# Kernel tuning notes

Hardware: AMD Instinct MI355X
Metric: run time of the kernel (lower is better)

## Reference

```python
import jax, jax.numpy as jnp
import numpy as np

HIDDEN = 512
IN_DIM = 512
N_ACT = 64
N_AGENTS = 8


def kalei_linear(x, ids, W, b, t):
    """x: [N, I]; ids: [N]; W: [O, I]; b: [O]; t: [A, O, I] -> [N, O].
    w_a = sign(W) * relu(|W| - sigmoid(t_a)); y_n = w_{ids[n]} @ x_n + b.
    """
    Wm = jnp.sign(W)[None] * jax.nn.relu(jnp.abs(W)[None] - jax.nn.sigmoid(t))  # [A,O,I]
    y = jnp.einsum('aoi,ni->nao', Wm, x)          # [N, A, O] batched masked GEMM
    y = jnp.take_along_axis(y, ids[:, None, None], axis=1)[:, 0]  # [N, O]
    return y + b[None, :]


def gru_cell(x, h, w_ih, w_hh, b_ih, b_hh):
    gi = x @ w_ih.T + b_ih
    gh = h @ w_hh.T + b_hh
    i_r, i_z, i_n = jnp.split(gi, 3, axis=-1)
    h_r, h_z, h_n = jnp.split(gh, 3, axis=-1)
    r = jax.nn.sigmoid(i_r + h_r)
    z = jax.nn.sigmoid(i_z + h_z)
    n = jnp.tanh(i_n + r * h_n)
    return (1.0 - z) * n + z * h


def setup_inputs() -> dict:
    key = jax.random.key(0)
    ks = jax.random.split(key, 20)
    B, A = 2048, N_AGENTS
    scale_init_lo, scale_init_hi = 3.0, 4.0  # -(rand*scale + bias) in [-4, -3]

    def thr(k, o, i):
        return -jax.random.uniform(k, (A, o, i), jnp.float32, scale_init_lo, scale_init_hi)

    w_scale = 0.05
    inp = {
        'inputs': jax.random.normal(ks[0], (B, A, IN_DIM), jnp.float32),
        'hidden_state': jax.random.normal(ks[1], (B, A, HIDDEN), jnp.float32),
        'agent_ids': jax.random.randint(ks[2], (B, A), 0, A),
        'fc1_w': jax.random.normal(ks[3], (HIDDEN, IN_DIM), jnp.float32) * w_scale,
        'fc1_b': jax.random.normal(ks[4], (HIDDEN,), jnp.float32) * w_scale,
        'fc1_t': thr(ks[5], HIDDEN, IN_DIM),
        'gru_wih': jax.random.normal(ks[6], (3 * HIDDEN, HIDDEN), jnp.float32) * w_scale,
        'gru_whh': jax.random.normal(ks[7], (3 * HIDDEN, HIDDEN), jnp.float32) * w_scale,
        'gru_bih': jax.random.normal(ks[8], (3 * HIDDEN,), jnp.float32) * w_scale,
        'gru_bhh': jax.random.normal(ks[9], (3 * HIDDEN,), jnp.float32) * w_scale,
        'fc2_w': jax.random.normal(ks[10], (HIDDEN, HIDDEN), jnp.float32) * w_scale,
        'fc2_b': jax.random.normal(ks[11], (HIDDEN,), jnp.float32) * w_scale,
        'fc2_t': thr(ks[12], HIDDEN, HIDDEN),
        'fc3_w': jax.random.normal(ks[13], (HIDDEN, HIDDEN), jnp.float32) * w_scale,
        'fc3_b': jax.random.normal(ks[14], (HIDDEN,), jnp.float32) * w_scale,
        'fc3_t': thr(ks[15], HIDDEN, HIDDEN),
        'fc4_w': jax.random.normal(ks[16], (N_ACT, HIDDEN), jnp.float32) * w_scale,
        'fc4_b': jax.random.normal(ks[17], (N_ACT,), jnp.float32) * w_scale,
        'fc4_t': thr(ks[18], N_ACT, HIDDEN),
    }
    return inp


def reference(inputs, hidden_state, agent_ids,
              fc1_w, fc1_b, fc1_t,
              gru_wih, gru_whh, gru_bih, gru_bhh,
              fc2_w, fc2_b, fc2_t,
              fc3_w, fc3_b, fc3_t,
              fc4_w, fc4_b, fc4_t):
    b, a, e = inputs.shape
    x = inputs.reshape(-1, e)                  # [N, e]
    ids = agent_ids.reshape(-1)                # [N]
    h_in = hidden_state.reshape(-1, HIDDEN)    # [N, H]

    x = jax.nn.relu(kalei_linear(x, ids, fc1_w, fc1_b, fc1_t))
    h = gru_cell(x, h_in, gru_wih, gru_whh, gru_bih, gru_bhh)
    q = jax.nn.relu(kalei_linear(h, ids, fc2_w, fc2_b, fc2_t))
    q = jax.nn.relu(kalei_linear(q, ids, fc3_w, fc3_b, fc3_t))
    q = kalei_linear(q, ids, fc4_w, fc4_b, fc4_t)
    return q.reshape(b, a, -1), h.reshape(b, a, -1)
```

## Files before the change

kernel.cpp:

```cpp
#include <hip/hip_runtime.h>
#include <hip/hip_bf16.h>
#include <stdint.h>

#define HID 512
#define NACT 64
#define NAG 8
#define NR 16384
#define BMT 128
#define MAXTILES 136

typedef __bf16 bf16_t;
typedef __bf16 bf16x4 __attribute__((ext_vector_type(4)));
typedef __bf16 bf16x8 __attribute__((ext_vector_type(8)));
typedef float  f32x16 __attribute__((ext_vector_type(16)));

#define MFMA32(a,b,c) __builtin_amdgcn_mfma_f32_32x32x16_bf16((a),(b),(c),0,0,0)

#define OFF_META 0
#define OFF_PERM 4096
#define OFF_WM1  (128*1024)
#define OFF_WM2  (OFF_WM1 + NAG*HID*HID*2)
#define OFF_WM3  (OFF_WM2 + NAG*HID*HID*2)
#define OFF_WM4  (OFF_WM3 + NAG*HID*HID*2)
#define OFF_WIH  (OFF_WM4 + NAG*NACT*HID*2)
#define OFF_WHH  (OFF_WIH + 3*HID*HID*2)
#define OFF_BUFA (OFF_WHH + 3*HID*HID*2)
#define OFF_BUFB (OFF_BUFA + (size_t)NR*HID*2)

__device__ inline void load_lds16(const void* g, void* l) {
  __builtin_amdgcn_global_load_lds((__attribute__((address_space(1))) void*)g,
                                   (__attribute__((address_space(3))) void*)l,
                                   16, 0, 0);
}

__device__ inline bf16x8 lds_frag(const bf16_t* base, int r, int cb) {
  return *(const bf16x8*)((const char*)base + r*128 + ((cb*16) ^ ((r&7)<<4)));
}

__device__ inline void store8bf(void* dst, float4 a, float4 b) {
  union { bf16_t h[8]; uint4 u; } p;
  p.h[0]=(bf16_t)a.x; p.h[1]=(bf16_t)a.y; p.h[2]=(bf16_t)a.z; p.h[3]=(bf16_t)a.w;
  p.h[4]=(bf16_t)b.x; p.h[5]=(bf16_t)b.y; p.h[6]=(bf16_t)b.z; p.h[7]=(bf16_t)b.w;
  *(uint4*)dst = p.u;
}

__device__ inline float kmask(float w, float t) {
  float s = 1.f / (1.f + __expf(-t));
  float m = fabsf(w) - s;
  return m > 0.f ? copysignf(m, w) : 0.f;
}

__device__ inline float sigm(float x) { return 1.f / (1.f + __expf(-x)); }
__device__ inline float tanh_f(float x) {
  float e = __expf(2.f * fabsf(x));
  return copysignf(1.f - 2.f/(e + 1.f), x);
}

__global__ void k_prep(const float* __restrict__ f1w, const float* __restrict__ f1t,
                       const float* __restrict__ f2w, const float* __restrict__ f2t,
                       const float* __restrict__ f3w, const float* __restrict__ f3t,
                       const float* __restrict__ f4w, const float* __restrict__ f4t,
                       const float* __restrict__ gih, const float* __restrict__ ghh,
                       bf16_t* __restrict__ wm1, bf16_t* __restrict__ wm2,
                       bf16_t* __restrict__ wm3, bf16_t* __restrict__ wm4,
                       bf16_t* __restrict__ wihb, bf16_t* __restrict__ whhb,
                       int* __restrict__ meta)
{
  const int tid = threadIdx.x;
  if (blockIdx.x == 0 && tid < 32) meta[tid] = 0;
  long v = (long)blockIdx.x * 256 + tid;
  const long VR1 = 524288;
  if (v < 3*VR1) {
    int which = (int)(v / VR1);
    long e = (v - (long)which*VR1) * 4;
    const float* W = which==0 ? f1w : (which==1 ? f2w : f3w);
    const float* T = which==0 ? f1t : (which==1 ? f2t : f3t);
    bf16_t* O = which==0 ? wm1 : (which==1 ? wm2 : wm3);
    long oi = e & (long)(HID*HID - 1);
    float4 w = *(const float4*)(W + oi);
    float4 t = *(const float4*)(T + e);
    bf16x4 o;
    o[0]=(bf16_t)kmask(w.x,t.x); o[1]=(bf16_t)kmask(w.y,t.y);
    o[2]=(bf16_t)kmask(w.z,t.z); o[3]=(bf16_t)kmask(w.w,t.w);
    *(bf16x4*)(O + e) = o;
  } else if (v < 3*VR1 + 65536) {
    long e = (v - 3*VR1) * 4;
    long oi = e & (long)(NACT*HID - 1);
    float4 w = *(const float4*)(f4w + oi);
    float4 t = *(const float4*)(f4t + e);
    bf16x4 o;
    o[0]=(bf16_t)kmask(w.x,t.x); o[1]=(bf16_t)kmask(w.y,t.y);
    o[2]=(bf16_t)kmask(w.z,t.z); o[3]=(bf16_t)kmask(w.w,t.w);
    *(bf16x4*)(wm4 + e) = o;
  } else if (v < 3*VR1 + 65536 + 196608) {
    long e = (v - (3*VR1 + 65536)) * 4;
    float4 x = *(const float4*)(gih + e);
    bf16x4 o; o[0]=(bf16_t)x.x; o[1]=(bf16_t)x.y; o[2]=(bf16_t)x.z; o[3]=(bf16_t)x.w;
    *(bf16x4*)(wihb + e) = o;
  } else if (v < 3*VR1 + 65536 + 2*196608) {
    long e = (v - (3*VR1 + 65536 + 196608)) * 4;
    float4 x = *(const float4*)(ghh + e);
    bf16x4 o; o[0]=(bf16_t)x.x; o[1]=(bf16_t)x.y; o[2]=(bf16_t)x.z; o[3]=(bf16_t)x.w;
    *(bf16x4*)(whhb + e) = o;
  }
}

__global__ void k_count(const int* __restrict__ ids, int* __restrict__ meta) {
  int n = blockIdx.x*256 + threadIdx.x;
  atomicAdd(&meta[ids[n]], 1);
}

__global__ void k_td(int* __restrict__ meta) {
  if (threadIdx.x != 0 || blockIdx.x != 0) return;
  int off = 0, nt = 0;
  for (int a = 0; a < NAG; ++a) {
    int c = meta[a];
    meta[8+a] = off;
    for (int t = 0; t*BMT < c; ++t) {
      meta[32 + nt]  = off + t*BMT;
      meta[192 + nt] = (c - t*BMT < BMT) ? (c - t*BMT) : BMT;
      meta[352 + nt] = a;
      ++nt;
    }
    off += c;
  }
  meta[16] = nt;
}

__global__ void k_scatter(const int* __restrict__ ids, int* __restrict__ meta,
                          int* __restrict__ perm) {
  int n = blockIdx.x*256 + threadIdx.x;
  int a = ids[n];
  int pos = atomicAdd(&meta[8+a], 1);
  perm[pos] = n;
}

template<int BN, int OTOT, bool GATHER, int OUTMODE>
__global__ __launch_bounds__(256)
void k_fc(const float* __restrict__ a_f32, const bf16_t* __restrict__ a_bf,
          const bf16_t* __restrict__ wbase, const float* __restrict__ bias,
          bf16_t* __restrict__ out_bf, float* __restrict__ out_f32,
          const int* __restrict__ meta, const int* __restrict__ perm)
{
  constexpr int FN = BN/64;
  const int bx = blockIdx.x;
  if (bx >= meta[16]) return;
  const int m0    = meta[32 + bx];
  const int rows  = meta[192 + bx];
  const int agent = meta[352 + bx];
  const int o0 = blockIdx.y * BN;
  const bf16_t* W = wbase + (size_t)agent * OTOT * HID;

  __shared__ bf16_t lA[BMT*64];
  __shared__ bf16_t lB[BN*64];

  const int tid = threadIdx.x, lane = tid & 63, wid = tid >> 6;
  const int wrow = wid & 1, wcol = wid >> 1;

  f32x16 zero;
  #pragma unroll
  for (int i = 0; i < 16; ++i) zero[i] = 0.f;
  f32x16 acc[2][FN];
  #pragma unroll
  for (int i = 0; i < 2; ++i)
    #pragma unroll
    for (int j = 0; j < FN; ++j) acc[i][j] = zero;

  for (int kp = 0; kp < HID/64; ++kp) {
    const int k0 = kp * 64;
    __syncthreads();
    if constexpr (GATHER) {
      #pragma unroll
      for (int it = 0; it < 4; ++it) {
        int t = it*256 + tid;
        int r = t >> 3, cb = t & 7;
        int rl = r < rows-1 ? r : rows-1;
        const float* sp = a_f32 + (size_t)perm[m0+rl]*HID + k0 + cb*8;
        float4 v0 = ((const float4*)sp)[0];
        float4 v1 = ((const float4*)sp)[1];
        store8bf((char*)lA + r*128 + ((cb*16) ^ ((r&7)<<4)), v0, v1);
      }
    } else {
      #pragma unroll
      for (int q = 0; q < 4; ++q) {
        int i = wid*4 + q;
        int r = i*8 + (lane>>3);
        int rl = r < rows-1 ? r : rows-1;
        int g = (lane&7) ^ ((lane>>3)&7);
        load_lds16(a_bf + (size_t)(m0+rl)*HID + k0 + g*8, (char*)lA + i*1024);
      }
    }
    #pragma unroll
    for (int q = 0; q < BN/32; ++q) {
      int i = wid*(BN/32) + q;
      int r = i*8 + (lane>>3);
      int g = (lane&7) ^ ((lane>>3)&7);
      load_lds16(W + (size_t)(o0+r)*HID + k0 + g*8, (char*)lB + i*1024);
    }
    __syncthreads();
    #pragma unroll
    for (int kk = 0; kk < 4; ++kk) {
      const int cbb = kk*2 + (lane>>5);
      bf16x8 af[2];
      #pragma unroll
      for (int fm = 0; fm < 2; ++fm) {
        int r = wrow*64 + fm*32 + (lane&31);
        af[fm] = lds_frag(lA, r, cbb);
      }
      #pragma unroll
      for (int fn = 0; fn < FN; ++fn) {
        int r = wcol*(BN/2) + fn*32 + (lane&31);
        bf16x8 bfv = lds_frag(lB, r, cbb);
        #pragma unroll
        for (int fm = 0; fm < 2; ++fm)
          acc[fm][fn] = MFMA32(af[fm], bfv, acc[fm][fn]);
      }
    }
  }

  #pragma unroll
  for (int fn = 0; fn < FN; ++fn) {
    int col = o0 + wcol*(BN/2) + fn*32 + (lane&31);
    float bv = bias[col];
    #pragma unroll
    for (int fm = 0; fm < 2; ++fm) {
      #pragma unroll
      for (int g = 0; g < 16; ++g) {
        int rl = wrow*64 + fm*32 + 4*(lane>>5) + (g&3) + 8*(g>>2);
        if (rl < rows) {
          float y = acc[fm][fn][g] + bv;
          if constexpr (OUTMODE == 0) {
            y = fmaxf(y, 0.f);
            out_bf[(size_t)(m0+rl)*OTOT + col] = (bf16_t)y;
          } else {
            out_f32[(size_t)perm[m0+rl]*OTOT + col] = y;
          }
        }
      }
    }
  }
}

__global__ __launch_bounds__(512)
void k_gru(const bf16_t* __restrict__ x1, const float* __restrict__ hidden,
           const bf16_t* __restrict__ wih, const bf16_t* __restrict__ whh,
           const float* __restrict__ bih, const float* __restrict__ bhh,
           bf16_t* __restrict__ hbuf, float* __restrict__ hout,
           const int* __restrict__ perm)
{
  const int m0 = blockIdx.x * BMT;
  const int j0 = blockIdx.y * 128;
  const int tid = threadIdx.x, lane = tid & 63, wid = tid >> 6;
  const int wrow = wid & 1, wcol = wid >> 1;

  __shared__ bf16_t lA[128*64];
  __shared__ bf16_t lB0[128*64];
  __shared__ bf16_t lB1[128*64];
  __shared__ bf16_t lB2[128*64];

  f32x16 zero;
  #pragma unroll
  for (int i = 0; i < 16; ++i) zero[i] = 0.f;
  f32x16 ar[2], az[2], an[2], ah[2];
  ar[0]=ar[1]=az[0]=az[1]=an[0]=an[1]=ah[0]=ah[1]=zero;

  for (int kp = 0; kp < 8; ++kp) {
    const int k0 = kp * 64;
    __syncthreads();
    #pragma unroll
    for (int q = 0; q < 2; ++q) {
      int i = wid*2 + q;
      int r = i*8 + (lane>>3);
      int g = (lane&7) ^ ((lane>>3)&7);
      load_lds16(x1  + (size_t)(m0+r)*HID        + k0 + g*8, (char*)lA  + i*1024);
      load_lds16(wih + (size_t)(j0+r)*HID        + k0 + g*8, (char*)lB0 + i*1024);
      load_lds16(wih + (size_t)(512+j0+r)*HID    + k0 + g*8, (char*)lB1 + i*1024);
      load_lds16(wih + (size_t)(1024+j0+r)*HID   + k0 + g*8, (char*)lB2 + i*1024);
    }
    __syncthreads();
    #pragma unroll
    for (int kk = 0; kk < 4; ++kk) {
      const int cbb = kk*2 + (lane>>5);
      bf16x8 af[2];
      #pragma unroll
      for (int fm = 0; fm < 2; ++fm)
        af[fm] = lds_frag(lA, wrow*64 + fm*32 + (lane&31), cbb);
      int rb = wcol*32 + (lane&31);
      bf16x8 b0 = lds_frag(lB0, rb, cbb);
      bf16x8 b1 = lds_frag(lB1, rb, cbb);
      bf16x8 b2 = lds_frag(lB2, rb, cbb);
      #pragma unroll
      for (int fm = 0; fm < 2; ++fm) {
        ar[fm] = MFMA32(af[fm], b0, ar[fm]);
        az[fm] = MFMA32(af[fm], b1, az[fm]);
        an[fm] = MFMA32(af[fm], b2, an[fm]);
      }
    }
  }
  for (int kp = 0; kp < 8; ++kp) {
    const int k0 = kp * 64;
    __syncthreads();
    #pragma unroll
    for (int it = 0; it < 2; ++it) {
      int t = it*512 + tid;
      int r = t >> 3, cb = t & 7;
      const float* sp = hidden + (size_t)perm[m0+r]*HID + k0 + cb*8;
      float4 v0 = ((const float4*)sp)[0];
      float4 v1 = ((const float4*)sp)[1];
      store8bf((char*)lA + r*128 + ((cb*16) ^ ((r&7)<<4)), v0, v1);
    }
    #pragma unroll
    for (int q = 0; q < 2; ++q) {
      int i = wid*2 + q;
      int r = i*8 + (lane>>3);
      int g = (lane&7) ^ ((lane>>3)&7);
      load_lds16(whh + (size_t)(j0+r)*HID      + k0 + g*8, (char*)lB0 + i*1024);
      load_lds16(whh + (size_t)(512+j0+r)*HID  + k0 + g*8, (char*)lB1 + i*1024);
      load_lds16(whh + (size_t)(1024+j0+r)*HID + k0 + g*8, (char*)lB2 + i*1024);
    }
    __syncthreads();
    #pragma unroll
    for (int kk = 0; kk < 4; ++kk) {
      const int cbb = kk*2 + (lane>>5);
      bf16x8 af[2];
      #pragma unroll
      for (int fm = 0; fm < 2; ++fm)
        af[fm] = lds_frag(lA, wrow*64 + fm*32 + (lane&31), cbb);
      int rb = wcol*32 + (lane&31);
      bf16x8 b0 = lds_frag(lB0, rb, cbb);
      bf16x8 b1 = lds_frag(lB1, rb, cbb);
      bf16x8 b2 = lds_frag(lB2, rb, cbb);
      #pragma unroll
      for (int fm = 0; fm < 2; ++fm) {
        ar[fm] = MFMA32(af[fm], b0, ar[fm]);
        az[fm] = MFMA32(af[fm], b1, az[fm]);
        ah[fm] = MFMA32(af[fm], b2, ah[fm]);
      }
    }
  }

  const int col = j0 + wcol*32 + (lane&31);
  const float b_r  = bih[col]        + bhh[col];
  const float b_z  = bih[512 + col]  + bhh[512 + col];
  const float b_in = bih[1024 + col];
  const float b_hn = bhh[1024 + col];
  #pragma unroll
  for (int fm = 0; fm < 2; ++fm) {
    #pragma unroll
    for (int g = 0; g < 16; ++g) {
      int rl = wrow*64 + fm*32 + 4*(lane>>5) + (g&3) + 8*(g>>2);
      int m = m0 + rl;
      int src = perm[m];
      float hp = hidden[(size_t)src*HID + col];
      float rg = sigm(ar[fm][g] + b_r);
      float zg = sigm(az[fm][g] + b_z);
      float ng = tanh_f(an[fm][g] + b_in + rg*(ah[fm][g] + b_hn));
      float h  = (1.f - zg)*ng + zg*hp;
      hbuf[(size_t)m*HID + col] = (bf16_t)h;
      hout[(size_t)src*HID + col] = h;
    }
  }
}

extern "C" void kernel_launch(void* const* d_in, const int* in_sizes, int n_in,
                              void* d_out, int out_size, void* d_ws, size_t ws_size,
                              hipStream_t stream) {
  const float* inputs  = (const float*)d_in[0];
  const float* hidden  = (const float*)d_in[1];
  const int*   ids     = (const int*)  d_in[2];
  const float* fc1_w   = (const float*)d_in[3];
  const float* fc1_b   = (const float*)d_in[4];
  const float* fc1_t   = (const float*)d_in[5];
  const float* gru_wih = (const float*)d_in[6];
  const float* gru_whh = (const float*)d_in[7];
  const float* gru_bih = (const float*)d_in[8];
  const float* gru_bhh = (const float*)d_in[9];
  const float* fc2_w   = (const float*)d_in[10];
  const float* fc2_b   = (const float*)d_in[11];
  const float* fc2_t   = (const float*)d_in[12];
  const float* fc3_w   = (const float*)d_in[13];
  const float* fc3_b   = (const float*)d_in[14];
  const float* fc3_t   = (const float*)d_in[15];
  const float* fc4_w   = (const float*)d_in[16];
  const float* fc4_b   = (const float*)d_in[17];
  const float* fc4_t   = (const float*)d_in[18];

  char* ws = (char*)d_ws;
  int*    meta = (int*)   (ws + OFF_META);
  int*    perm = (int*)   (ws + OFF_PERM);
  bf16_t* wm1  = (bf16_t*)(ws + OFF_WM1);
  bf16_t* wm2  = (bf16_t*)(ws + OFF_WM2);
  bf16_t* wm3  = (bf16_t*)(ws + OFF_WM3);
  bf16_t* wm4  = (bf16_t*)(ws + OFF_WM4);
  bf16_t* wihb = (bf16_t*)(ws + OFF_WIH);
  bf16_t* whhb = (bf16_t*)(ws + OFF_WHH);
  bf16_t* bufA = (bf16_t*)(ws + OFF_BUFA);
  bf16_t* bufB = (bf16_t*)(ws + OFF_BUFB);

  float* q_out = (float*)d_out;
  float* h_out = q_out + (size_t)NR * NACT;

  k_prep<<<7936, 256, 0, stream>>>(fc1_w, fc1_t, fc2_w, fc2_t, fc3_w, fc3_t,
                                   fc4_w, fc4_t, gru_wih, gru_whh,
                                   wm1, wm2, wm3, wm4, wihb, whhb, meta);
  k_count<<<64, 256, 0, stream>>>(ids, meta);
  k_td<<<1, 64, 0, stream>>>(meta);
  k_scatter<<<64, 256, 0, stream>>>(ids, meta, perm);

  k_fc<128, HID, true, 0><<<dim3(MAXTILES, 4), 256, 0, stream>>>(
      inputs, nullptr, wm1, fc1_b, bufA, nullptr, meta, perm);
  k_gru<<<dim3(NR/BMT, 4), 512, 0, stream>>>(bufA, hidden, wihb, whhb,
                                             gru_bih, gru_bhh, bufB, h_out, perm);
  k_fc<128, HID, false, 0><<<dim3(MAXTILES, 4), 256, 0, stream>>>(
      nullptr, bufB, wm2, fc2_b, bufA, nullptr, meta, perm);
  k_fc<128, HID, false, 0><<<dim3(MAXTILES, 4), 256, 0, stream>>>(
      nullptr, bufA, wm3, fc3_b, bufB, nullptr, meta, perm);
  k_fc<64, NACT, false, 1><<<dim3(MAXTILES, 1), 256, 0, stream>>>(
      nullptr, bufB, wm4, fc4_b, nullptr, q_out, meta, perm);
}
```

Before: 317.7 us.

## Pre-gather inputs to bf16 and double-buffer LDS loads in FC and GRU kernels

```diff
diff --git a/kernel.cpp b/kernel.cpp
--- a/kernel.cpp
+++ b/kernel.cpp
@@ -24,14 +24,23 @@
 #define OFF_WM4  (OFF_WM3 + NAG*HID*HID*2)
 #define OFF_WIH  (OFF_WM4 + NAG*NACT*HID*2)
 #define OFF_WHH  (OFF_WIH + 3*HID*HID*2)
-#define OFF_BUFA (OFF_WHH + 3*HID*HID*2)
-#define OFF_BUFB (OFF_BUFA + (size_t)NR*HID*2)
+#define OFF_XS   (OFF_WHH + 3*HID*HID*2)
+#define OFF_HS   (OFF_XS + (size_t)NR*HID*2)
+#define OFF_B1   (OFF_HS + (size_t)NR*HID*2)
 
 __device__ inline void load_lds16(const void* g, void* l) {
   __builtin_amdgcn_global_load_lds((__attribute__((address_space(1))) void*)g,
                                    (__attribute__((address_space(3))) void*)l,
                                    16, 0, 0);
 }
+
+template<int N> __device__ inline void wait_vmcnt() {
+  asm volatile("s_waitcnt vmcnt(%0)" :: "n"(N) : "memory");
+}
+__device__ inline void wait_lgkm0() {
+  asm volatile("s_waitcnt lgkmcnt(0)" ::: "memory");
+}
+#define BAR() __builtin_amdgcn_s_barrier()
 
 __device__ inline bf16x8 lds_frag(const bf16_t* base, int r, int cb) {
   return *(const bf16x8*)((const char*)base + r*128 + ((cb*16) ^ ((r&7)<<4)));
@@ -49,7 +58,6 @@
   float m = fabsf(w) - s;
   return m > 0.f ? copysignf(m, w) : 0.f;
 }
-
 __device__ inline float sigm(float x) { return 1.f / (1.f + __expf(-x)); }
 __device__ inline float tanh_f(float x) {
   float e = __expf(2.f * fabsf(x));
@@ -111,7 +119,6 @@
 }
 
 __global__ void k_td(int* __restrict__ meta) {
-  if (threadIdx.x != 0 || blockIdx.x != 0) return;
   int off = 0, nt = 0;
   for (int a = 0; a < NAG; ++a) {
     int c = meta[a];
@@ -135,27 +142,44 @@
   perm[pos] = n;
 }
 
-template<int BN, int OTOT, bool GATHER, int OUTMODE>
+__global__ void k_gather(const float* __restrict__ inputs, const float* __restrict__ hidden,
+                         const int* __restrict__ perm,
+                         bf16_t* __restrict__ xs, bf16_t* __restrict__ hs)
+{
+  int tid = threadIdx.x;
+  int rb = blockIdx.x*4 + (tid>>6);
+  int m = rb & (NR-1);
+  int src = perm[m];
+  const float* sp; bf16_t* op;
+  if (rb < NR) { sp = inputs + (size_t)src*HID; op = xs + (size_t)m*HID; }
+  else         { sp = hidden + (size_t)src*HID; op = hs + (size_t)m*HID; }
+  int c = (tid&63)*8;
+  float4 v0 = *(const float4*)(sp + c);
+  float4 v1 = *(const float4*)(sp + c + 4);
+  store8bf(op + c, v0, v1);
+}
+
+template<int BN, int OTOT, int OUTMODE>
 __global__ __launch_bounds__(256)
-void k_fc(const float* __restrict__ a_f32, const bf16_t* __restrict__ a_bf,
-          const bf16_t* __restrict__ wbase, const float* __restrict__ bias,
+void k_fc(const bf16_t* __restrict__ a_bf, const bf16_t* __restrict__ wbase,
+          const float* __restrict__ bias,
           bf16_t* __restrict__ out_bf, float* __restrict__ out_f32,
           const int* __restrict__ meta, const int* __restrict__ perm)
 {
-  constexpr int FN = BN/64;
+  constexpr int FN  = BN/64;
+  constexpr int NLB = BN/32;
+  constexpr int NLD = 4 + NLB;
   const int bx = blockIdx.x;
   if (bx >= meta[16]) return;
-  const int m0    = meta[32 + bx];
-  const int rows  = meta[192 + bx];
-  const int agent = meta[352 + bx];
+  const int m0 = meta[32+bx], rows = meta[192+bx], agent = meta[352+bx];
   const int o0 = blockIdx.y * BN;
   const bf16_t* W = wbase + (size_t)agent * OTOT * HID;
 
-  __shared__ bf16_t lA[BMT*64];
-  __shared__ bf16_t lB[BN*64];
+  __shared__ bf16_t lds[2][(BMT + BN)*64];
 
   const int tid = threadIdx.x, lane = tid & 63, wid = tid >> 6;
   const int wrow = wid & 1, wcol = wid >> 1;
+  const int gsw = (lane&7) ^ ((lane>>3)&7);
 
   f32x16 zero;
   #pragma unroll
@@ -166,57 +190,54 @@
     #pragma unroll
     for (int j = 0; j < FN; ++j) acc[i][j] = zero;
 
-  for (int kp = 0; kp < HID/64; ++kp) {
+  auto stage = [&](int kp, int s) {
     const int k0 = kp * 64;
-    __syncthreads();
-    if constexpr (GATHER) {
-      #pragma unroll
-      for (int it = 0; it < 4; ++it) {
-        int t = it*256 + tid;
-        int r = t >> 3, cb = t & 7;
-        int rl = r < rows-1 ? r : rows-1;
-        const float* sp = a_f32 + (size_t)perm[m0+rl]*HID + k0 + cb*8;
-        float4 v0 = ((const float4*)sp)[0];
-        float4 v1 = ((const float4*)sp)[1];
-        store8bf((char*)lA + r*128 + ((cb*16) ^ ((r&7)<<4)), v0, v1);
-      }
-    } else {
-      #pragma unroll
-      for (int q = 0; q < 4; ++q) {
-        int i = wid*4 + q;
-        int r = i*8 + (lane>>3);
-        int rl = r < rows-1 ? r : rows-1;
-        int g = (lane&7) ^ ((lane>>3)&7);
-        load_lds16(a_bf + (size_t)(m0+rl)*HID + k0 + g*8, (char*)lA + i*1024);
-      }
-    }
-    #pragma unroll
-    for (int q = 0; q < BN/32; ++q) {
-      int i = wid*(BN/32) + q;
+    bf16_t* LA = &lds[s][0];
+    bf16_t* LB = &lds[s][BMT*64];
+    #pragma unroll
+    for (int q = 0; q < 4; ++q) {
+      int i = wid*4 + q;
       int r = i*8 + (lane>>3);
-      int g = (lane&7) ^ ((lane>>3)&7);
-      load_lds16(W + (size_t)(o0+r)*HID + k0 + g*8, (char*)lB + i*1024);
-    }
-    __syncthreads();
+      int rl = r < rows ? r : rows-1;
+      load_lds16(a_bf + (size_t)(m0+rl)*HID + k0 + gsw*8, (char*)LA + i*1024);
+    }
+    #pragma unroll
+    for (int q = 0; q < NLB; ++q) {
+      int i = wid*NLB + q;
+      int r = i*8 + (lane>>3);
+      load_lds16(W + (size_t)(o0+r)*HID + k0 + gsw*8, (char*)LB + i*1024);
+    }
+  };
+
+  auto compute = [&](int s) {
+    const bf16_t* LA = &lds[s][0];
+    const bf16_t* LB = &lds[s][BMT*64];
     #pragma unroll
     for (int kk = 0; kk < 4; ++kk) {
       const int cbb = kk*2 + (lane>>5);
       bf16x8 af[2];
       #pragma unroll
-      for (int fm = 0; fm < 2; ++fm) {
-        int r = wrow*64 + fm*32 + (lane&31);
-        af[fm] = lds_frag(lA, r, cbb);
-      }
+      for (int fm = 0; fm < 2; ++fm)
+        af[fm] = lds_frag(LA, wrow*64 + fm*32 + (lane&31), cbb);
       #pragma unroll
       for (int fn = 0; fn < FN; ++fn) {
-        int r = wcol*(BN/2) + fn*32 + (lane&31);
-        bf16x8 bfv = lds_frag(lB, r, cbb);
+        bf16x8 bv = lds_frag(LB, wcol*(BN/2) + fn*32 + (lane&31), cbb);
         #pragma unroll
         for (int fm = 0; fm < 2; ++fm)
-          acc[fm][fn] = MFMA32(af[fm], bfv, acc[fm][fn]);
+          acc[fm][fn] = MFMA32(af[fm], bv, acc[fm][fn]);
       }
     }
-  }
+  };
+
+  stage(0, 0); stage(1, 1);
+  for (int t = 0; t < 6; ++t) {
+    wait_vmcnt<NLD>(); BAR();
+    compute(t & 1);
+    wait_lgkm0(); BAR();
+    stage(t + 2, t & 1);
+  }
+  wait_vmcnt<NLD>(); BAR(); compute(0); wait_lgkm0(); BAR();
+  wait_vmcnt<0>();   BAR(); compute(1);
 
   #pragma unroll
   for (int fn = 0; fn < FN; ++fn) {
@@ -241,22 +262,21 @@
   }
 }
 
-__global__ __launch_bounds__(512)
-void k_gru(const bf16_t* __restrict__ x1, const float* __restrict__ hidden,
+__global__ __launch_bounds__(256)
+void k_gru(const bf16_t* __restrict__ x1, const bf16_t* __restrict__ hs,
+           const float* __restrict__ hidden,
            const bf16_t* __restrict__ wih, const bf16_t* __restrict__ whh,
            const float* __restrict__ bih, const float* __restrict__ bhh,
            bf16_t* __restrict__ hbuf, float* __restrict__ hout,
            const int* __restrict__ perm)
 {
   const int m0 = blockIdx.x * BMT;
-  const int j0 = blockIdx.y * 128;
+  const int j0 = blockIdx.y * 64;
   const int tid = threadIdx.x, lane = tid & 63, wid = tid >> 6;
   const int wrow = wid & 1, wcol = wid >> 1;
-
-  __shared__ bf16_t lA[128*64];
-  __shared__ bf16_t lB0[128*64];
-  __shared__ bf16_t lB1[128*64];
-  __shared__ bf16_t lB2[128*64];
+  const int gsw = (lane&7) ^ ((lane>>3)&7);
+
+  __shared__ bf16_t lds[2][(BMT + 192)*64];
 
   f32x16 zero;
   #pragma unroll
@@ -264,80 +284,60 @@
   f32x16 ar[2], az[2], an[2], ah[2];
   ar[0]=ar[1]=az[0]=az[1]=an[0]=an[1]=ah[0]=ah[1]=zero;
 
-  for (int kp = 0; kp < 8; ++kp) {
-    const int k0 = kp * 64;
-    __syncthreads();
-    #pragma unroll
-    for (int q = 0; q < 2; ++q) {
-      int i = wid*2 + q;
+  auto stage = [&](int kp, int s) {
+    const bf16_t* A  = (kp < 8) ? x1  : hs;
+    const bf16_t* Wg = (kp < 8) ? wih : whh;
+    const int k0 = (kp & 7) * 64;
+    bf16_t* LA = &lds[s][0];
+    bf16_t* LB = &lds[s][BMT*64];
+    #pragma unroll
+    for (int q = 0; q < 4; ++q) {
+      int i = wid*4 + q;
       int r = i*8 + (lane>>3);
-      int g = (lane&7) ^ ((lane>>3)&7);
-      load_lds16(x1  + (size_t)(m0+r)*HID        + k0 + g*8, (char*)lA  + i*1024);
-      load_lds16(wih + (size_t)(j0+r)*HID        + k0 + g*8, (char*)lB0 + i*1024);
-      load_lds16(wih + (size_t)(512+j0+r)*HID    + k0 + g*8, (char*)lB1 + i*1024);
-      load_lds16(wih + (size_t)(1024+j0+r)*HID   + k0 + g*8, (char*)lB2 + i*1024);
-    }
-    __syncthreads();
+      load_lds16(A + (size_t)(m0+r)*HID + k0 + gsw*8, (char*)LA + i*1024);
+    }
+    #pragma unroll
+    for (int q = 0; q < 6; ++q) {
+      int i = wid*6 + q;
+      int gate = i >> 3, rb = i & 7;
+      int rr = gate*HID + j0 + rb*8 + (lane>>3);
+      load_lds16(Wg + (size_t)rr*HID + k0 + gsw*8, (char*)LB + i*1024);
+    }
+  };
+
+  auto compute = [&](int s, f32x16 (&a3)[2]) {
+    const bf16_t* LA = &lds[s][0];
+    const bf16_t* LB = &lds[s][BMT*64];
     #pragma unroll
     for (int kk = 0; kk < 4; ++kk) {
       const int cbb = kk*2 + (lane>>5);
-      bf16x8 af[2];
-      #pragma unroll
-      for (int fm = 0; fm < 2; ++fm)
-        af[fm] = lds_frag(lA, wrow*64 + fm*32 + (lane&31), cbb);
-      int rb = wcol*32 + (lane&31);
-      bf16x8 b0 = lds_frag(lB0, rb, cbb);
-      bf16x8 b1 = lds_frag(lB1, rb, cbb);
-      bf16x8 b2 = lds_frag(lB2, rb, cbb);
-      #pragma unroll
-      for (int fm = 0; fm < 2; ++fm) {
-        ar[fm] = MFMA32(af[fm], b0, ar[fm]);
-        az[fm] = MFMA32(af[fm], b1, az[fm]);
-        an[fm] = MFMA32(af[fm], b2, an[fm]);
-      }
-    }
-  }
-  for (int kp = 0; kp < 8; ++kp) {
-    const int k0 = kp * 64;
-    __syncthreads();
-    #pragma unroll
-    for (int it = 0; it < 2; ++it) {
-      int t = it*512 + tid;
-      int r = t >> 3, cb = t & 7;
-      const float* sp = hidden + (size_t)perm[m0+r]*HID + k0 + cb*8;
-      float4 v0 = ((const float4*)sp)[0];
-      float4 v1 = ((const float4*)sp)[1];
-      store8bf((char*)lA + r*128 + ((cb*16) ^ ((r&7)<<4)), v0, v1);
-    }
-    #pragma unroll
-    for (int q = 0; q < 2; ++q) {
-      int i = wid*2 + q;
-      int r = i*8 + (lane>>3);
-      int g = (lane&7) ^ ((lane>>3)&7);
-      load_lds16(whh + (size_t)(j0+r)*HID      + k0 + g*8, (char*)lB0 + i*1024);
-      load_lds16(whh + (size_t)(512+j0+r)*HID  + k0 + g*8, (char*)lB1 + i*1024);
-      load_lds16(whh + (size_t)(1024+j0+r)*HID + k0 + g*8, (char*)lB2 + i*1024);
-    }
-    __syncthreads();
-    #pragma unroll
-    for (int kk = 0; kk < 4; ++kk) {
-      const int cbb = kk*2 + (lane>>5);
-      bf16x8 af[2];
-      #pragma unroll
-      for (int fm = 0; fm < 2; ++fm)
-        af[fm] = lds_frag(lA, wrow*64 + fm*32 + (lane&31), cbb);
-      int rb = wcol*32 + (lane&31);
-      bf16x8 b0 = lds_frag(lB0, rb, cbb);
-      bf16x8 b1 = lds_frag(lB1, rb, cbb);
-      bf16x8 b2 = lds_frag(lB2, rb, cbb);
-      #pragma unroll
-      for (int fm = 0; fm < 2; ++fm) {
-        ar[fm] = MFMA32(af[fm], b0, ar[fm]);
-        az[fm] = MFMA32(af[fm], b1, az[fm]);
-        ah[fm] = MFMA32(af[fm], b2, ah[fm]);
-      }
-    }
-  }
+      bf16x8 af0 = lds_frag(LA, wrow*64 +      (lane&31), cbb);
+      bf16x8 af1 = lds_frag(LA, wrow*64 + 32 + (lane&31), cbb);
+      const int rb = wcol*32 + (lane&31);
+      bf16x8 b0 = lds_frag(LB,        rb, cbb);
+      bf16x8 b1 = lds_frag(LB + 4096, rb, cbb);
+      bf16x8 b2 = lds_frag(LB + 8192, rb, cbb);
+      ar[0] = MFMA32(af0, b0, ar[0]); ar[1] = MFMA32(af1, b0, ar[1]);
+      az[0] = MFMA32(af0, b1, az[0]); az[1] = MFMA32(af1, b1, az[1]);
+      a3[0] = MFMA32(af0, b2, a3[0]); a3[1] = MFMA32(af1, b2, a3[1]);
+    }
+  };
+
+  stage(0, 0); stage(1, 1);
+  for (int t = 0; t < 8; ++t) {
+    wait_vmcnt<10>(); BAR();
+    compute(t & 1, an);
+    wait_lgkm0(); BAR();
+    stage(t + 2, t & 1);
+  }
+  for (int t = 8; t < 14; ++t) {
+    wait_vmcnt<10>(); BAR();
+    compute(t & 1, ah);
+    wait_lgkm0(); BAR();
+    stage(t + 2, t & 1);
+  }
+  wait_vmcnt<10>(); BAR(); compute(0, ah); wait_lgkm0(); BAR();
+  wait_vmcnt<0>();  BAR(); compute(1, ah);
 
   const int col = j0 + wcol*32 + (lane&31);
   const float b_r  = bih[col]        + bhh[col];
@@ -394,8 +394,9 @@
   bf16_t* wm4  = (bf16_t*)(ws + OFF_WM4);
   bf16_t* wihb = (bf16_t*)(ws + OFF_WIH);
   bf16_t* whhb = (bf16_t*)(ws + OFF_WHH);
-  bf16_t* bufA = (bf16_t*)(ws + OFF_BUFA);
-  bf16_t* bufB = (bf16_t*)(ws + OFF_BUFB);
+  bf16_t* xs   = (bf16_t*)(ws + OFF_XS);
+  bf16_t* hs   = (bf16_t*)(ws + OFF_HS);
+  bf16_t* b1   = (bf16_t*)(ws + OFF_B1);
 
   float* q_out = (float*)d_out;
   float* h_out = q_out + (size_t)NR * NACT;
@@ -404,17 +405,18 @@
                                    fc4_w, fc4_t, gru_wih, gru_whh,
                                    wm1, wm2, wm3, wm4, wihb, whhb, meta);
   k_count<<<64, 256, 0, stream>>>(ids, meta);
-  k_td<<<1, 64, 0, stream>>>(meta);
+  k_td<<<1, 1, 0, stream>>>(meta);
   k_scatter<<<64, 256, 0, stream>>>(ids, meta, perm);
-
-  k_fc<128, HID, true, 0><<<dim3(MAXTILES, 4), 256, 0, stream>>>(
-      inputs, nullptr, wm1, fc1_b, bufA, nullptr, meta, perm);
-  k_gru<<<dim3(NR/BMT, 4), 512, 0, stream>>>(bufA, hidden, wihb, whhb,
-                                             gru_bih, gru_bhh, bufB, h_out, perm);
-  k_fc<128, HID, false, 0><<<dim3(MAXTILES, 4), 256, 0, stream>>>(
-      nullptr, bufB, wm2, fc2_b, bufA, nullptr, meta, perm);
-  k_fc<128, HID, false, 0><<<dim3(MAXTILES, 4), 256, 0, stream>>>(
-      nullptr, bufA, wm3, fc3_b, bufB, nullptr, meta, perm);
-  k_fc<64, NACT, false, 1><<<dim3(MAXTILES, 1), 256, 0, stream>>>(
-      nullptr, bufB, wm4, fc4_b, nullptr, q_out, meta, perm);
-}
+  k_gather<<<8192, 256, 0, stream>>>(inputs, hidden, perm, xs, hs);
+
+  k_fc<128, HID, 0><<<dim3(MAXTILES, 4), 256, 0, stream>>>(
+      xs, wm1, fc1_b, b1, nullptr, meta, perm);
+  k_gru<<<dim3(NR/BMT, 8), 256, 0, stream>>>(b1, hs, hidden, wihb, whhb,
+                                             gru_bih, gru_bhh, xs, h_out, perm);
+  k_fc<128, HID, 0><<<dim3(MAXTILES, 4), 256, 0, stream>>>(
+      xs, wm2, fc2_b, b1, nullptr, meta, perm);
+  k_fc<128, HID, 0><<<dim3(MAXTILES, 4), 256, 0, stream>>>(
+      b1, wm3, fc3_b, hs, nullptr, meta, perm);
+  k_fc<64, NACT, 1><<<dim3(MAXTILES, 1), 256, 0, stream>>>(
+      hs, wm4, fc4_b, nullptr, q_out, meta, perm);
+}
```

Measured after the change: 330.2 us. 3.9% more time.
